# Kernel optimization log

Measured on AMD Instinct MI355X. Metric: run time of the kernel, lower is better.

Reference implementation:

```python
import jax, jax.numpy as jnp
import numpy as np

EPS = 1e-5


def _gcn_conv(h, W, b, src, dst, norm, N):
    # h: (B, N, F_in) -> linear transform then normalized neighbor aggregation
    h = h @ W                                  # (B, N, H)
    msg = h[:, src, :] * norm[None, :, None]   # gather + edge norm, (B, E, H)
    agg = jax.vmap(lambda m: jax.ops.segment_sum(m, dst, num_segments=N))(msg)
    return agg + b


def _batchnorm(h, gamma, beta):
    # BatchNorm1d over flattened (B*N, H), training-mode batch statistics
    B, N, H = h.shape
    f = h.reshape(-1, H)
    mean = f.mean(axis=0)
    var = f.var(axis=0)
    f = (f - mean) * jax.lax.rsqrt(var + EPS) * gamma + beta
    return f.reshape(B, N, H)


def setup_inputs() -> dict:
    key = jax.random.key(0)
    ks = jax.random.split(key, 6)
    B, N, E, IN, H, OUT = 2, 20000, 640000, 128, 128, 10
    x = jax.random.normal(ks[0], (B, N, IN), dtype=jnp.float32)
    edge_index = jax.random.randint(ks[1], (2, E), 0, N, dtype=jnp.int64)
    W1 = jax.random.normal(ks[2], (IN, H), dtype=jnp.float32) / np.sqrt(IN)
    W2 = jax.random.normal(ks[3], (H, H), dtype=jnp.float32) / np.sqrt(H)
    Wc = jax.random.normal(ks[4], (H, OUT), dtype=jnp.float32) / np.sqrt(H)
    return {
        "x": x,
        "W1": W1, "b1": jnp.zeros((H,), jnp.float32),
        "W2": W2, "b2": jnp.zeros((H,), jnp.float32),
        "g1": jnp.ones((H,), jnp.float32), "bt1": jnp.zeros((H,), jnp.float32),
        "g2": jnp.ones((H,), jnp.float32), "bt2": jnp.zeros((H,), jnp.float32),
        "Wc": Wc, "bc": jnp.zeros((OUT,), jnp.float32),
        "edge_index": edge_index,
    }


def reference(x, W1, b1, W2, b2, g1, bt1, g2, bt2, Wc, bc, edge_index):
    N = x.shape[1]
    loops = jnp.arange(N, dtype=edge_index.dtype)
    src = jnp.concatenate([edge_index[0], loops])  # add self-loops (GCNConv default)
    dst = jnp.concatenate([edge_index[1], loops])
    deg = jax.ops.segment_sum(jnp.ones(src.shape[0], x.dtype), dst, num_segments=N)
    dinv = jnp.where(deg > 0, jax.lax.rsqrt(deg), 0.0)
    norm = dinv[src] * dinv[dst]                   # symmetric GCN normalization

    h = jax.nn.relu(_gcn_conv(x, W1, b1, src, dst, norm, N))
    h = _batchnorm(h, g1, bt1)
    # dropout is identity in eval mode
    h = jax.nn.relu(_gcn_conv(h, W2, b2, src, dst, norm, N))
    h = _batchnorm(h, g2, bt2)
    return h @ Wc + bc                              # (B, N, out_dim)
```

## Files before the change

### kernel.cpp

```cpp
#include <hip/hip_runtime.h>
#include <hip/hip_bf16.h>


constexpr int Nn   = 20000;
constexpr int Ee   = 640000;
constexpr int OUTd = 10;
constexpr int Mm   = 2 * Nn;
constexpr int ELLW = 96;
constexpr int NSLOT = 64;
constexpr int NP   = 8;
constexpr int PSZ  = Nn / NP;
constexpr int PCAP = 98304;
constexpr int GMB  = Mm / 64;
constexpr int BKB  = (Ee + 1023) / 1024;
constexpr int PBB  = 96;
#define EPSV 1e-5f
constexpr float INV_M = 1.0f / (float)Mm;

using frag16 = __attribute__((ext_vector_type(8))) short;
using f32x4  = __attribute__((ext_vector_type(4))) float;

__device__ inline short bf(float f) {
    union { __hip_bfloat16 h; short s; } u;
    u.h = __float2bfloat16(f);
    return u.s;
}
__device__ inline float lo16(unsigned u) { union { unsigned v; float f; } x; x.v = u << 16;        return x.f; }
__device__ inline float hi16(unsigned u) { union { unsigned v; float f; } x; x.v = u & 0xffff0000u; return x.f; }
__device__ inline unsigned pack2(float f0, float f1) {
    return (unsigned)(unsigned short)bf(f0) | ((unsigned)(unsigned short)bf(f1) << 16);
}
__device__ inline float wdeg(int c) { return rsqrtf((float)c + 1.0f); }

__global__ __launch_bounds__(256) void fg1_k(const int* __restrict__ src, const int* __restrict__ dst,
                                             int* __restrict__ cursor, uint2* __restrict__ pairs,
                                             const float* __restrict__ A,
                                             const float* __restrict__ W,
                                             unsigned short* __restrict__ Hout) {
    __shared__ short Wl[128 * 136];
    __shared__ int pcnt[NP];
    __shared__ int pbase[NP];
    int t = threadIdx.x;

    if (blockIdx.x >= GMB) {
        int s  = blockIdx.x - GMB;
        int e0 = s * 1024;
        if (t < NP) pcnt[t] = 0;
        __syncthreads();
        int es[4], ed[4], pp[4], pos[4];
        #pragma unroll
        for (int it = 0; it < 4; ++it) {
            int e = e0 + it * 256 + t;
            int d = dst[e];
            es[it] = src[e];
            ed[it] = d;
            pp[it] = (int)((unsigned)d / (unsigned)PSZ);
            pos[it] = atomicAdd(&pcnt[pp[it]], 1);
        }
        __syncthreads();
        if (t < NP) pbase[t] = atomicAdd(&cursor[t], pcnt[t]);
        __syncthreads();
        #pragma unroll
        for (int it = 0; it < 4; ++it) {
            int idx = pbase[pp[it]] + pos[it];
            if (idx < PCAP)
                pairs[(size_t)pp[it] * PCAP + idx] = make_uint2((unsigned)es[it], (unsigned)ed[it]);
        }
        return;
    }

    int bid = blockIdx.x;

    for (int it = 0; it < 8; ++it) {
        int lin = it * 256 + t;
        int kp  = lin & 63;
        int n4  = (lin >> 6) * 4;
        float4 w0 = *(const float4*)(W + (size_t)(2 * kp) * 128 + n4);
        float4 w1 = *(const float4*)(W + (size_t)(2 * kp + 1) * 128 + n4);
        *(unsigned*)&Wl[(n4 + 0) * 136 + 2 * kp] = pack2(w0.x, w1.x);
        *(unsigned*)&Wl[(n4 + 1) * 136 + 2 * kp] = pack2(w0.y, w1.y);
        *(unsigned*)&Wl[(n4 + 2) * 136 + 2 * kp] = pack2(w0.z, w1.z);
        *(unsigned*)&Wl[(n4 + 3) * 136 + 2 * kp] = pack2(w0.w, w1.w);
    }
    __syncthreads();

    int wv = t >> 6, l = t & 63;
    int row_q = l >> 4, lane16 = l & 15;
    int row0 = bid * 64 + wv * 16;

    frag16 a[4];
    const float* Arow = A + (size_t)(row0 + lane16) * 128;
    #pragma unroll
    for (int q = 0; q < 4; ++q) {
        int k0 = q * 32 + row_q * 8;
        float4 v0 = *(const float4*)(Arow + k0);
        float4 v1 = *(const float4*)(Arow + k0 + 4);
        frag16 fa = { bf(v0.x), bf(v0.y), bf(v0.z), bf(v0.w),
                      bf(v1.x), bf(v1.y), bf(v1.z), bf(v1.w) };
        a[q] = fa;
    }

    f32x4 acc[8];
    #pragma unroll
    for (int c = 0; c < 8; ++c) acc[c] = (f32x4){0.f, 0.f, 0.f, 0.f};

    #pragma unroll
    for (int c = 0; c < 8; ++c) {
        int n = c * 16 + lane16;
        #pragma unroll
        for (int q = 0; q < 4; ++q) {
            int k0 = q * 32 + row_q * 8;
            frag16 b = *(const frag16*)&Wl[n * 136 + k0];
            acc[c] = __builtin_amdgcn_mfma_f32_16x16x32_bf16(a[q], b, acc[c], 0, 0, 0);
        }
    }

    #pragma unroll
    for (int r = 0; r < 4; ++r) {
        int rg = row0 + row_q * 4 + r;
        int b  = rg >= Nn;
        int n  = rg - b * Nn;
        unsigned short* dstp = Hout + (size_t)n * 256 + b * 128;
        #pragma unroll
        for (int c = 0; c < 8; ++c)
            dstp[c * 16 + lane16] = (unsigned short)bf(acc[c][r]);
    }
}

__global__ __launch_bounds__(256) void scat2_k(const uint2* __restrict__ pairs,
                                               const int* __restrict__ cursor,
                                               int* __restrict__ cnt, int* __restrict__ ell) {
    int p     = blockIdx.x & (NP - 1);
    int chunk = blockIdx.x >> 3;
    int m = cursor[p]; if (m > PCAP) m = PCAP;
    const uint2* bk = pairs + (size_t)p * PCAP;
    for (int i = chunk * 256 + threadIdx.x; i < m; i += PBB * 256) {
        uint2 pr = bk[i];
        int d = (int)pr.y;
        int pos = atomicAdd(&cnt[d], 1);
        if (pos < ELLW) ell[(size_t)d * ELLW + pos] = (int)pr.x;
    }
}

__global__ __launch_bounds__(256) void gemm2_k(const unsigned short* __restrict__ Abf,
                                               const float* __restrict__ W,
                                               const float* __restrict__ g,
                                               const float* __restrict__ bt,
                                               const float* __restrict__ S,
                                               const int* __restrict__ cnt,
                                               unsigned short* __restrict__ Hout) {
    __shared__ short Wl[128 * 136];
    __shared__ float al[128], cl[128], dpart[2][128];
    int t = threadIdx.x;

    if (t < 128) {
        float s = 0.f, ss = 0.f;
        #pragma unroll 8
        for (int k = 0; k < NSLOT; ++k) {
            s  += S[k * 256 + t];
            ss += S[k * 256 + 128 + t];
        }
        float m   = s * INV_M;
        float var = ss * INV_M - m * m;
        float a   = g[t] * rsqrtf(var + EPSV);
        float c   = bt[t] - m * a;
        al[t] = a; cl[t] = c;
    }
    __syncthreads();

    for (int it = 0; it < 8; ++it) {
        int lin = it * 256 + t;
        int kp  = lin & 63;
        int n4  = (lin >> 6) * 4;
        float a0 = al[2 * kp], a1 = al[2 * kp + 1];
        float4 w0 = *(const float4*)(W + (size_t)(2 * kp) * 128 + n4);
        float4 w1 = *(const float4*)(W + (size_t)(2 * kp + 1) * 128 + n4);
        w0.x *= a0; w0.y *= a0; w0.z *= a0; w0.w *= a0;
        w1.x *= a1; w1.y *= a1; w1.z *= a1; w1.w *= a1;
        *(unsigned*)&Wl[(n4 + 0) * 136 + 2 * kp] = pack2(w0.x, w1.x);
        *(unsigned*)&Wl[(n4 + 1) * 136 + 2 * kp] = pack2(w0.y, w1.y);
        *(unsigned*)&Wl[(n4 + 2) * 136 + 2 * kp] = pack2(w0.z, w1.z);
        *(unsigned*)&Wl[(n4 + 3) * 136 + 2 * kp] = pack2(w0.w, w1.w);
    }

    {
        int col = t & 127, hh = t >> 7;
        const float* Wc0 = W + (size_t)(hh * 64) * 128 + col;
        float dp = 0.f;
        #pragma unroll 8
        for (int k = 0; k < 64; ++k) dp += cl[hh * 64 + k] * Wc0[(size_t)k * 128];
        dpart[hh][col] = dp;
    }
    __syncthreads();

    int wv = t >> 6, l = t & 63;
    int row_q = l >> 4, lane16 = l & 15;
    int row0 = blockIdx.x * 64 + wv * 16;

    int rgA = row0 + lane16;
    int bA  = rgA >= Nn;
    int nA  = rgA - bA * Nn;
    const unsigned short* Arow = Abf + (size_t)nA * 256 + bA * 128;
    frag16 a[4];
    #pragma unroll
    for (int q = 0; q < 4; ++q) {
        int k0 = q * 32 + row_q * 8;
        a[q] = *(const frag16*)(Arow + k0);
    }

    f32x4 acc[8];
    #pragma unroll
    for (int c = 0; c < 8; ++c) {
        int n = c * 16 + lane16;
        float d = dpart[0][n] + dpart[1][n];
        acc[c] = (f32x4){d, d, d, d};
    }

    #pragma unroll
    for (int c = 0; c < 8; ++c) {
        int n = c * 16 + lane16;
        #pragma unroll
        for (int q = 0; q < 4; ++q) {
            int k0 = q * 32 + row_q * 8;
            frag16 b = *(const frag16*)&Wl[n * 136 + k0];
            acc[c] = __builtin_amdgcn_mfma_f32_16x16x32_bf16(a[q], b, acc[c], 0, 0, 0);
        }
    }

    #pragma unroll
    for (int r = 0; r < 4; ++r) {
        int rg = row0 + row_q * 4 + r;
        int b  = rg >= Nn;
        int n  = rg - b * Nn;
        float dv = wdeg(cnt[n]);
        unsigned short* dst = Hout + (size_t)n * 256 + b * 128;
        #pragma unroll
        for (int c = 0; c < 8; ++c)
            dst[c * 16 + lane16] = (unsigned short)bf(acc[c][r] * dv);
    }
}

template<int WEIGHTED>
__global__ __launch_bounds__(256) void aggs_k(const unsigned short* __restrict__ h,
                                              const int* __restrict__ ell,
                                              const int* __restrict__ cnt,
                                              const float* __restrict__ bias,
                                              unsigned short* __restrict__ act,
                                              float* __restrict__ S) {
    int t    = threadIdx.x;
    int wv   = t >> 6;
    int l    = t & 63;
    int p    = blockIdx.x & 7;
    int ng   = blockIdx.x >> 3;
    int esub = l >> 2;
    int c4   = l & 3;
    int uo   = p * 4 + c4;
    const uint4* h4 = (const uint4*)h;
    int cb   = (p & 3) * 32 + c4 * 8;

    float oS[8] = {0.f,0.f,0.f,0.f,0.f,0.f,0.f,0.f};
    float qS[8] = {0.f,0.f,0.f,0.f,0.f,0.f,0.f,0.f};

    for (int s = 0; s < 2; ++s) {
        int n = __builtin_amdgcn_readfirstlane(ng * 8 + wv * 2 + s);
        int degc = cnt[n];
        float dn = wdeg(degc);
        int deg = degc > ELLW ? ELLW : degc;
        const int* row = ell + (size_t)n * ELLW;

        uint4 u = h4[(size_t)n * 32 + uo];

        float a0 = 0.f, a1 = 0.f, a2 = 0.f, a3 = 0.f;
        float a4 = 0.f, a5 = 0.f, a6 = 0.f, a7 = 0.f;

        int j = 0;
        for (; j + 32 <= deg; j += 32) {
            int i0 = row[j + esub];
            int i1 = row[j + 16 + esub];
            float w0 = 1.f, w1 = 1.f;
            if (WEIGHTED) { w0 = wdeg(cnt[i0]); w1 = wdeg(cnt[i1]); }
            uint4 v0 = h4[(size_t)i0 * 32 + uo];
            uint4 v1 = h4[(size_t)i1 * 32 + uo];
            if (WEIGHTED) {
                a0 = fmaf(w0, lo16(v0.x), a0); a1 = fmaf(w0, hi16(v0.x), a1);
                a2 = fmaf(w0, lo16(v0.y), a2); a3 = fmaf(w0, hi16(v0.y), a3);
                a4 = fmaf(w0, lo16(v0.z), a4); a5 = fmaf(w0, hi16(v0.z), a5);
                a6 = fmaf(w0, lo16(v0.w), a6); a7 = fmaf(w0, hi16(v0.w), a7);
                a0 = fmaf(w1, lo16(v1.x), a0); a1 = fmaf(w1, hi16(v1.x), a1);
                a2 = fmaf(w1, lo16(v1.y), a2); a3 = fmaf(w1, hi16(v1.y), a3);
                a4 = fmaf(w1, lo16(v1.z), a4); a5 = fmaf(w1, hi16(v1.z), a5);
                a6 = fmaf(w1, lo16(v1.w), a6); a7 = fmaf(w1, hi16(v1.w), a7);
            } else {
                a0 += lo16(v0.x); a1 += hi16(v0.x); a2 += lo16(v0.y); a3 += hi16(v0.y);
                a4 += lo16(v0.z); a5 += hi16(v0.z); a6 += lo16(v0.w); a7 += hi16(v0.w);
                a0 += lo16(v1.x); a1 += hi16(v1.x); a2 += lo16(v1.y); a3 += hi16(v1.y);
                a4 += lo16(v1.z); a5 += hi16(v1.z); a6 += lo16(v1.w); a7 += hi16(v1.w);
            }
        }
        for (; j + 16 <= deg; j += 16) {
            int i0 = row[j + esub];
            float w0 = 1.f;
            if (WEIGHTED) w0 = wdeg(cnt[i0]);
            uint4 v0 = h4[(size_t)i0 * 32 + uo];
            if (WEIGHTED) {
                a0 = fmaf(w0, lo16(v0.x), a0); a1 = fmaf(w0, hi16(v0.x), a1);
                a2 = fmaf(w0, lo16(v0.y), a2); a3 = fmaf(w0, hi16(v0.y), a3);
                a4 = fmaf(w0, lo16(v0.z), a4); a5 = fmaf(w0, hi16(v0.z), a5);
                a6 = fmaf(w0, lo16(v0.w), a6); a7 = fmaf(w0, hi16(v0.w), a7);
            } else {
                a0 += lo16(v0.x); a1 += hi16(v0.x); a2 += lo16(v0.y); a3 += hi16(v0.y);
                a4 += lo16(v0.z); a5 += hi16(v0.z); a6 += lo16(v0.w); a7 += hi16(v0.w);
            }
        }
        if (j < deg) {
            int e = j + esub;
            if (e < deg) {
                int i0 = row[e];
                float w0 = 1.f;
                if (WEIGHTED) w0 = wdeg(cnt[i0]);
                uint4 v0 = h4[(size_t)i0 * 32 + uo];
                if (WEIGHTED) {
                    a0 = fmaf(w0, lo16(v0.x), a0); a1 = fmaf(w0, hi16(v0.x), a1);
                    a2 = fmaf(w0, lo16(v0.y), a2); a3 = fmaf(w0, hi16(v0.y), a3);
                    a4 = fmaf(w0, lo16(v0.z), a4); a5 = fmaf(w0, hi16(v0.z), a5);
                    a6 = fmaf(w0, lo16(v0.w), a6); a7 = fmaf(w0, hi16(v0.w), a7);
                } else {
                    a0 += lo16(v0.x); a1 += hi16(v0.x); a2 += lo16(v0.y); a3 += hi16(v0.y);
                    a4 += lo16(v0.z); a5 += hi16(v0.z); a6 += lo16(v0.w); a7 += hi16(v0.w);
                }
            }
        }

        #pragma unroll
        for (int m = 4; m <= 32; m <<= 1) {
            a0 += __shfl_xor(a0, m); a1 += __shfl_xor(a1, m);
            a2 += __shfl_xor(a2, m); a3 += __shfl_xor(a3, m);
            a4 += __shfl_xor(a4, m); a5 += __shfl_xor(a5, m);
            a6 += __shfl_xor(a6, m); a7 += __shfl_xor(a7, m);
        }

        if (l < 4) {
            float4 b0 = *(const float4*)(bias + cb);
            float4 b1 = *(const float4*)(bias + cb + 4);
            float o0, o1, o2, o3, o4, o5, o6, o7;
            if (WEIGHTED) {
                o0 = fmaxf(fmaf(dn, fmaf(dn, lo16(u.x), a0), b0.x), 0.f);
                o1 = fmaxf(fmaf(dn, fmaf(dn, hi16(u.x), a1), b0.y), 0.f);
                o2 = fmaxf(fmaf(dn, fmaf(dn, lo16(u.y), a2), b0.z), 0.f);
                o3 = fmaxf(fmaf(dn, fmaf(dn, hi16(u.y), a3), b0.w), 0.f);
                o4 = fmaxf(fmaf(dn, fmaf(dn, lo16(u.z), a4), b1.x), 0.f);
                o5 = fmaxf(fmaf(dn, fmaf(dn, hi16(u.z), a5), b1.y), 0.f);
                o6 = fmaxf(fmaf(dn, fmaf(dn, lo16(u.w), a6), b1.z), 0.f);
                o7 = fmaxf(fmaf(dn, fmaf(dn, hi16(u.w), a7), b1.w), 0.f);
            } else {
                o0 = fmaxf(fmaf(dn, a0 + lo16(u.x), b0.x), 0.f);
                o1 = fmaxf(fmaf(dn, a1 + hi16(u.x), b0.y), 0.f);
                o2 = fmaxf(fmaf(dn, a2 + lo16(u.y), b0.z), 0.f);
                o3 = fmaxf(fmaf(dn, a3 + hi16(u.y), b0.w), 0.f);
                o4 = fmaxf(fmaf(dn, a4 + lo16(u.z), b1.x), 0.f);
                o5 = fmaxf(fmaf(dn, a5 + hi16(u.z), b1.y), 0.f);
                o6 = fmaxf(fmaf(dn, a6 + lo16(u.w), b1.z), 0.f);
                o7 = fmaxf(fmaf(dn, a7 + hi16(u.w), b1.w), 0.f);
            }
            uint4 st;
            st.x = pack2(o0, o1); st.y = pack2(o2, o3);
            st.z = pack2(o4, o5); st.w = pack2(o6, o7);
            *(uint4*)(act + (size_t)n * 256 + (size_t)p * 32 + (size_t)c4 * 8) = st;

            oS[0] += o0; oS[1] += o1; oS[2] += o2; oS[3] += o3;
            oS[4] += o4; oS[5] += o5; oS[6] += o6; oS[7] += o7;
            qS[0] += o0*o0; qS[1] += o1*o1; qS[2] += o2*o2; qS[3] += o3*o3;
            qS[4] += o4*o4; qS[5] += o5*o5; qS[6] += o6*o6; qS[7] += o7*o7;
        }
    }

    __shared__ float sh[4][4][16];
    if (l < 4) {
        float* ptr = sh[wv][l];
        #pragma unroll
        for (int k = 0; k < 8; ++k) { ptr[k] = oS[k]; ptr[8 + k] = qS[k]; }
    }
    __syncthreads();
    if (t < 64) {
        int c = t >> 4;
        int k = t & 15;
        float v = sh[0][c][k] + sh[1][c][k] + sh[2][c][k] + sh[3][c][k];
        int col  = (p & 3) * 32 + c * 8 + (k & 7);
        int stat = k >> 3;
        atomicAdd(&S[((blockIdx.x >> 3) & (NSLOT - 1)) * 256 + stat * 128 + col], v);
    }
}

__global__ __launch_bounds__(256) void gemmout_k(const unsigned short* __restrict__ act,
                                                 const float* __restrict__ Wc,
                                                 const float* __restrict__ bc,
                                                 const float* __restrict__ g,
                                                 const float* __restrict__ bt,
                                                 const float* __restrict__ S,
                                                 float* __restrict__ out) {
    __shared__ float Wl[128 * OUTd];
    __shared__ float bl[OUTd];
    __shared__ float al[128], cl[128];
    int t = threadIdx.x;
    for (int i = t; i < 128 * OUTd; i += 256) Wl[i] = Wc[i];
    if (t < OUTd) bl[t] = bc[t];
    if (t < 128) {
        float s = 0.f, ss = 0.f;
        #pragma unroll 8
        for (int k = 0; k < NSLOT; ++k) {
            s  += S[k * 256 + t];
            ss += S[k * 256 + 128 + t];
        }
        float m   = s * INV_M;
        float var = ss * INV_M - m * m;
        float a   = g[t] * rsqrtf(var + EPSV);
        al[t] = a;
        cl[t] = bt[t] - m * a;
    }
    __syncthreads();

    int r = blockIdx.x * 256 + t;
    if (r >= Mm) return;
    int b = r >= Nn;
    int n = r - b * Nn;

    float acc[OUTd];
    #pragma unroll
    for (int jj = 0; jj < OUTd; jj++) acc[jj] = 0.f;

    const uint4* a4 = (const uint4*)(act + (size_t)n * 256 + b * 128);
    #pragma unroll 4
    for (int k4 = 0; k4 < 16; k4++) {
        uint4 u = a4[k4];
        int k = k4 * 8;
        float e0 = lo16(u.x) * al[k+0] + cl[k+0];
        float e1 = hi16(u.x) * al[k+1] + cl[k+1];
        float e2 = lo16(u.y) * al[k+2] + cl[k+2];
        float e3 = hi16(u.y) * al[k+3] + cl[k+3];
        float e4 = lo16(u.z) * al[k+4] + cl[k+4];
        float e5 = hi16(u.z) * al[k+5] + cl[k+5];
        float e6 = lo16(u.w) * al[k+6] + cl[k+6];
        float e7 = hi16(u.w) * al[k+7] + cl[k+7];
        #pragma unroll
        for (int jj = 0; jj < OUTd; jj++) {
            acc[jj] += e0 * Wl[(k+0) * OUTd + jj];
            acc[jj] += e1 * Wl[(k+1) * OUTd + jj];
            acc[jj] += e2 * Wl[(k+2) * OUTd + jj];
            acc[jj] += e3 * Wl[(k+3) * OUTd + jj];
            acc[jj] += e4 * Wl[(k+4) * OUTd + jj];
            acc[jj] += e5 * Wl[(k+5) * OUTd + jj];
            acc[jj] += e6 * Wl[(k+6) * OUTd + jj];
            acc[jj] += e7 * Wl[(k+7) * OUTd + jj];
        }
    }
    #pragma unroll
    for (int jj = 0; jj < OUTd; jj++) out[(size_t)r * OUTd + jj] = acc[jj] + bl[jj];
}

extern "C" void kernel_launch(void* const* d_in, const int* in_sizes, int n_in,
                              void* d_out, int out_size, void* d_ws, size_t ws_size,
                              hipStream_t stream) {
    (void)in_sizes; (void)n_in; (void)out_size; (void)ws_size;

    const float* x   = (const float*)d_in[0];
    const float* W1  = (const float*)d_in[1];
    const float* b1  = (const float*)d_in[2];
    const float* W2  = (const float*)d_in[3];
    const float* b2  = (const float*)d_in[4];
    const float* g1  = (const float*)d_in[5];
    const float* bt1 = (const float*)d_in[6];
    const float* g2  = (const float*)d_in[7];
    const float* bt2 = (const float*)d_in[8];
    const float* Wc  = (const float*)d_in[9];
    const float* bc  = (const float*)d_in[10];
    const int*   ei  = (const int*)d_in[11];
    const int* srcp = ei;
    const int* dstp = ei + Ee;

    char* ws = (char*)d_ws;
    size_t off = 0;
    auto alloc = [&](size_t bytes) -> void* {
        void* p = ws + off;
        off += (bytes + 511) & ~(size_t)511;
        return p;
    };
    unsigned short* h   = (unsigned short*)alloc((size_t)Mm * 128 * 2);
    unsigned short* act = (unsigned short*)alloc((size_t)Mm * 128 * 2);
    int*   cnt  = (int*)alloc(Nn * 4 + 2 * NSLOT * 256 * 4 + NP * 4);
    float* S1   = (float*)(cnt + Nn);
    float* S2   = S1 + NSLOT * 256;
    int*   cursor = (int*)(S2 + NSLOT * 256);
    int*   ell  = (int*)alloc((size_t)Nn * ELLW * 4);
    uint2* pairs = (uint2*)alloc((size_t)NP * PCAP * 8);

    float* out = (float*)d_out;

    hipMemsetAsync(cnt, 0, Nn * 4 + 2 * NSLOT * 256 * 4 + NP * 4, stream);
    fg1_k<<<GMB + BKB, 256, 0, stream>>>(srcp, dstp, cursor, pairs, x, W1, h);

    scat2_k<<<NP * PBB, 256, 0, stream>>>(pairs, cursor, cnt, ell);

    aggs_k<1><<<(Nn / 8) * 8, 256, 0, stream>>>(h, ell, cnt, b1, act, S1);

    gemm2_k<<<Mm / 64, 256, 0, stream>>>(act, W2, g1, bt1, S1, cnt, h);
    aggs_k<0><<<(Nn / 8) * 8, 256, 0, stream>>>(h, ell, cnt, b2, act, S2);

    gemmout_k<<<(Mm + 255) / 256, 256, 0, stream>>>(act, Wc, bc, g2, bt2, S2, out);
}
```

Before: 296.5 us.

## Remap aggregation warps to one node and 64 columns each, unroll edge loop

Reworks the SpMM aggregation kernel so each block splits its 256 columns into 4 parts instead of 8, with each warp owning one node and 8 lanes spanning 64 bf16 columns (128 bytes per neighbor row). The edge loop now issues four gathers per iteration instead of two. The aim is fewer, wider gather transactions per neighbor, fewer redundant index loads across blocks, and more memory-level parallelism. In exchange each block handles fewer nodes, there is one more shuffle-free lane group, and per-block stats atomics roughly double in count.

```diff
diff --git a/kernel.cpp b/kernel.cpp
--- a/kernel.cpp
+++ b/kernel.cpp
@@ -240,6 +240,17 @@
     }
 }
 
+#define ACCW8(V, W) \
+    a0 = fmaf(W, lo16((V).x), a0); a1 = fmaf(W, hi16((V).x), a1); \
+    a2 = fmaf(W, lo16((V).y), a2); a3 = fmaf(W, hi16((V).y), a3); \
+    a4 = fmaf(W, lo16((V).z), a4); a5 = fmaf(W, hi16((V).z), a5); \
+    a6 = fmaf(W, lo16((V).w), a6); a7 = fmaf(W, hi16((V).w), a7);
+#define ACC8(V) \
+    a0 += lo16((V).x); a1 += hi16((V).x); \
+    a2 += lo16((V).y); a3 += hi16((V).y); \
+    a4 += lo16((V).z); a5 += hi16((V).z); \
+    a6 += lo16((V).w); a7 += hi16((V).w);
+
 template<int WEIGHTED>
 __global__ __launch_bounds__(256) void aggs_k(const unsigned short* __restrict__ h,
                                               const int* __restrict__ ell,
@@ -247,147 +258,110 @@
                                               const float* __restrict__ bias,
                                               unsigned short* __restrict__ act,
                                               float* __restrict__ S) {
-    int t    = threadIdx.x;
-    int wv   = t >> 6;
-    int l    = t & 63;
-    int p    = blockIdx.x & 7;
-    int ng   = blockIdx.x >> 3;
-    int esub = l >> 2;
-    int c4   = l & 3;
-    int uo   = p * 4 + c4;
+    int t  = threadIdx.x;
+    int wv = t >> 6;
+    int l  = t & 63;
+    int p  = blockIdx.x & 3;
+    int ng = blockIdx.x >> 2;
+    int n  = __builtin_amdgcn_readfirstlane(ng * 4 + wv);
+    int c  = l & 7;
+    int eo = l >> 3;
+    int uo = p * 8 + c;
     const uint4* h4 = (const uint4*)h;
-    int cb   = (p & 3) * 32 + c4 * 8;
-
-    float oS[8] = {0.f,0.f,0.f,0.f,0.f,0.f,0.f,0.f};
-    float qS[8] = {0.f,0.f,0.f,0.f,0.f,0.f,0.f,0.f};
-
-    for (int s = 0; s < 2; ++s) {
-        int n = __builtin_amdgcn_readfirstlane(ng * 8 + wv * 2 + s);
-        int degc = cnt[n];
-        float dn = wdeg(degc);
-        int deg = degc > ELLW ? ELLW : degc;
-        const int* row = ell + (size_t)n * ELLW;
-
-        uint4 u = h4[(size_t)n * 32 + uo];
-
-        float a0 = 0.f, a1 = 0.f, a2 = 0.f, a3 = 0.f;
-        float a4 = 0.f, a5 = 0.f, a6 = 0.f, a7 = 0.f;
-
-        int j = 0;
-        for (; j + 32 <= deg; j += 32) {
-            int i0 = row[j + esub];
-            int i1 = row[j + 16 + esub];
-            float w0 = 1.f, w1 = 1.f;
-            if (WEIGHTED) { w0 = wdeg(cnt[i0]); w1 = wdeg(cnt[i1]); }
-            uint4 v0 = h4[(size_t)i0 * 32 + uo];
-            uint4 v1 = h4[(size_t)i1 * 32 + uo];
-            if (WEIGHTED) {
-                a0 = fmaf(w0, lo16(v0.x), a0); a1 = fmaf(w0, hi16(v0.x), a1);
-                a2 = fmaf(w0, lo16(v0.y), a2); a3 = fmaf(w0, hi16(v0.y), a3);
-                a4 = fmaf(w0, lo16(v0.z), a4); a5 = fmaf(w0, hi16(v0.z), a5);
-                a6 = fmaf(w0, lo16(v0.w), a6); a7 = fmaf(w0, hi16(v0.w), a7);
-                a0 = fmaf(w1, lo16(v1.x), a0); a1 = fmaf(w1, hi16(v1.x), a1);
-                a2 = fmaf(w1, lo16(v1.y), a2); a3 = fmaf(w1, hi16(v1.y), a3);
-                a4 = fmaf(w1, lo16(v1.z), a4); a5 = fmaf(w1, hi16(v1.z), a5);
-                a6 = fmaf(w1, lo16(v1.w), a6); a7 = fmaf(w1, hi16(v1.w), a7);
-            } else {
-                a0 += lo16(v0.x); a1 += hi16(v0.x); a2 += lo16(v0.y); a3 += hi16(v0.y);
-                a4 += lo16(v0.z); a5 += hi16(v0.z); a6 += lo16(v0.w); a7 += hi16(v0.w);
-                a0 += lo16(v1.x); a1 += hi16(v1.x); a2 += lo16(v1.y); a3 += hi16(v1.y);
-                a4 += lo16(v1.z); a5 += hi16(v1.z); a6 += lo16(v1.w); a7 += hi16(v1.w);
-            }
-        }
-        for (; j + 16 <= deg; j += 16) {
-            int i0 = row[j + esub];
-            float w0 = 1.f;
-            if (WEIGHTED) w0 = wdeg(cnt[i0]);
-            uint4 v0 = h4[(size_t)i0 * 32 + uo];
-            if (WEIGHTED) {
-                a0 = fmaf(w0, lo16(v0.x), a0); a1 = fmaf(w0, hi16(v0.x), a1);
-                a2 = fmaf(w0, lo16(v0.y), a2); a3 = fmaf(w0, hi16(v0.y), a3);
-                a4 = fmaf(w0, lo16(v0.z), a4); a5 = fmaf(w0, hi16(v0.z), a5);
-                a6 = fmaf(w0, lo16(v0.w), a6); a7 = fmaf(w0, hi16(v0.w), a7);
-            } else {
-                a0 += lo16(v0.x); a1 += hi16(v0.x); a2 += lo16(v0.y); a3 += hi16(v0.y);
-                a4 += lo16(v0.z); a5 += hi16(v0.z); a6 += lo16(v0.w); a7 += hi16(v0.w);
-            }
-        }
-        if (j < deg) {
-            int e = j + esub;
-            if (e < deg) {
-                int i0 = row[e];
-                float w0 = 1.f;
-                if (WEIGHTED) w0 = wdeg(cnt[i0]);
-                uint4 v0 = h4[(size_t)i0 * 32 + uo];
-                if (WEIGHTED) {
-                    a0 = fmaf(w0, lo16(v0.x), a0); a1 = fmaf(w0, hi16(v0.x), a1);
-                    a2 = fmaf(w0, lo16(v0.y), a2); a3 = fmaf(w0, hi16(v0.y), a3);
-                    a4 = fmaf(w0, lo16(v0.z), a4); a5 = fmaf(w0, hi16(v0.z), a5);
-                    a6 = fmaf(w0, lo16(v0.w), a6); a7 = fmaf(w0, hi16(v0.w), a7);
-                } else {
-                    a0 += lo16(v0.x); a1 += hi16(v0.x); a2 += lo16(v0.y); a3 += hi16(v0.y);
-                    a4 += lo16(v0.z); a5 += hi16(v0.z); a6 += lo16(v0.w); a7 += hi16(v0.w);
-                }
-            }
-        }
-
-        #pragma unroll
-        for (int m = 4; m <= 32; m <<= 1) {
-            a0 += __shfl_xor(a0, m); a1 += __shfl_xor(a1, m);
-            a2 += __shfl_xor(a2, m); a3 += __shfl_xor(a3, m);
-            a4 += __shfl_xor(a4, m); a5 += __shfl_xor(a5, m);
-            a6 += __shfl_xor(a6, m); a7 += __shfl_xor(a7, m);
-        }
-
-        if (l < 4) {
-            float4 b0 = *(const float4*)(bias + cb);
-            float4 b1 = *(const float4*)(bias + cb + 4);
-            float o0, o1, o2, o3, o4, o5, o6, o7;
-            if (WEIGHTED) {
-                o0 = fmaxf(fmaf(dn, fmaf(dn, lo16(u.x), a0), b0.x), 0.f);
-                o1 = fmaxf(fmaf(dn, fmaf(dn, hi16(u.x), a1), b0.y), 0.f);
-                o2 = fmaxf(fmaf(dn, fmaf(dn, lo16(u.y), a2), b0.z), 0.f);
-                o3 = fmaxf(fmaf(dn, fmaf(dn, hi16(u.y), a3), b0.w), 0.f);
-                o4 = fmaxf(fmaf(dn, fmaf(dn, lo16(u.z), a4), b1.x), 0.f);
-                o5 = fmaxf(fmaf(dn, fmaf(dn, hi16(u.z), a5), b1.y), 0.f);
-                o6 = fmaxf(fmaf(dn, fmaf(dn, lo16(u.w), a6), b1.z), 0.f);
-                o7 = fmaxf(fmaf(dn, fmaf(dn, hi16(u.w), a7), b1.w), 0.f);
-            } else {
-                o0 = fmaxf(fmaf(dn, a0 + lo16(u.x), b0.x), 0.f);
-                o1 = fmaxf(fmaf(dn, a1 + hi16(u.x), b0.y), 0.f);
-                o2 = fmaxf(fmaf(dn, a2 + lo16(u.y), b0.z), 0.f);
-                o3 = fmaxf(fmaf(dn, a3 + hi16(u.y), b0.w), 0.f);
-                o4 = fmaxf(fmaf(dn, a4 + lo16(u.z), b1.x), 0.f);
-                o5 = fmaxf(fmaf(dn, a5 + hi16(u.z), b1.y), 0.f);
-                o6 = fmaxf(fmaf(dn, a6 + lo16(u.w), b1.z), 0.f);
-                o7 = fmaxf(fmaf(dn, a7 + hi16(u.w), b1.w), 0.f);
-            }
-            uint4 st;
-            st.x = pack2(o0, o1); st.y = pack2(o2, o3);
-            st.z = pack2(o4, o5); st.w = pack2(o6, o7);
-            *(uint4*)(act + (size_t)n * 256 + (size_t)p * 32 + (size_t)c4 * 8) = st;
-
-            oS[0] += o0; oS[1] += o1; oS[2] += o2; oS[3] += o3;
-            oS[4] += o4; oS[5] += o5; oS[6] += o6; oS[7] += o7;
-            qS[0] += o0*o0; qS[1] += o1*o1; qS[2] += o2*o2; qS[3] += o3*o3;
-            qS[4] += o4*o4; qS[5] += o5*o5; qS[6] += o6*o6; qS[7] += o7*o7;
-        }
-    }
-
-    __shared__ float sh[4][4][16];
-    if (l < 4) {
+
+    int degc = cnt[n];
+    float dn = wdeg(degc);
+    int deg = degc > ELLW ? ELLW : degc;
+    const int* row = ell + (size_t)n * ELLW;
+
+    uint4 u = h4[(size_t)n * 32 + uo];
+
+    float a0 = 0.f, a1 = 0.f, a2 = 0.f, a3 = 0.f;
+    float a4 = 0.f, a5 = 0.f, a6 = 0.f, a7 = 0.f;
+
+    int j = 0;
+    for (; j + 32 <= deg; j += 32) {
+        int i0 = row[j      + eo];
+        int i1 = row[j +  8 + eo];
+        int i2 = row[j + 16 + eo];
+        int i3 = row[j + 24 + eo];
+        uint4 v0 = h4[(size_t)i0 * 32 + uo];
+        uint4 v1 = h4[(size_t)i1 * 32 + uo];
+        uint4 v2 = h4[(size_t)i2 * 32 + uo];
+        uint4 v3 = h4[(size_t)i3 * 32 + uo];
+        if (WEIGHTED) {
+            float w0 = wdeg(cnt[i0]), w1 = wdeg(cnt[i1]);
+            float w2 = wdeg(cnt[i2]), w3 = wdeg(cnt[i3]);
+            ACCW8(v0, w0); ACCW8(v1, w1); ACCW8(v2, w2); ACCW8(v3, w3);
+        } else {
+            ACC8(v0); ACC8(v1); ACC8(v2); ACC8(v3);
+        }
+    }
+    for (; j + 8 <= deg; j += 8) {
+        int i0 = row[j + eo];
+        uint4 v0 = h4[(size_t)i0 * 32 + uo];
+        if (WEIGHTED) { float w0 = wdeg(cnt[i0]); ACCW8(v0, w0); }
+        else          { ACC8(v0); }
+    }
+    if (j + eo < deg) {
+        int i0 = row[j + eo];
+        uint4 v0 = h4[(size_t)i0 * 32 + uo];
+        if (WEIGHTED) { float w0 = wdeg(cnt[i0]); ACCW8(v0, w0); }
+        else          { ACC8(v0); }
+    }
+
+    #pragma unroll
+    for (int m = 8; m <= 32; m <<= 1) {
+        a0 += __shfl_xor(a0, m); a1 += __shfl_xor(a1, m);
+        a2 += __shfl_xor(a2, m); a3 += __shfl_xor(a3, m);
+        a4 += __shfl_xor(a4, m); a5 += __shfl_xor(a5, m);
+        a6 += __shfl_xor(a6, m); a7 += __shfl_xor(a7, m);
+    }
+
+    __shared__ float sh[4][8][16];
+    if (l < 8) {
+        int colbase = (p & 1) * 64 + l * 8;
+        float4 b0 = *(const float4*)(bias + colbase);
+        float4 b1 = *(const float4*)(bias + colbase + 4);
+        float o0, o1, o2, o3, o4, o5, o6, o7;
+        if (WEIGHTED) {
+            o0 = fmaxf(fmaf(dn, fmaf(dn, lo16(u.x), a0), b0.x), 0.f);
+            o1 = fmaxf(fmaf(dn, fmaf(dn, hi16(u.x), a1), b0.y), 0.f);
+            o2 = fmaxf(fmaf(dn, fmaf(dn, lo16(u.y), a2), b0.z), 0.f);
+            o3 = fmaxf(fmaf(dn, fmaf(dn, hi16(u.y), a3), b0.w), 0.f);
+            o4 = fmaxf(fmaf(dn, fmaf(dn, lo16(u.z), a4), b1.x), 0.f);
+            o5 = fmaxf(fmaf(dn, fmaf(dn, hi16(u.z), a5), b1.y), 0.f);
+            o6 = fmaxf(fmaf(dn, fmaf(dn, lo16(u.w), a6), b1.z), 0.f);
+            o7 = fmaxf(fmaf(dn, fmaf(dn, hi16(u.w), a7), b1.w), 0.f);
+        } else {
+            o0 = fmaxf(fmaf(dn, a0 + lo16(u.x), b0.x), 0.f);
+            o1 = fmaxf(fmaf(dn, a1 + hi16(u.x), b0.y), 0.f);
+            o2 = fmaxf(fmaf(dn, a2 + lo16(u.y), b0.z), 0.f);
+            o3 = fmaxf(fmaf(dn, a3 + hi16(u.y), b0.w), 0.f);
+            o4 = fmaxf(fmaf(dn, a4 + lo16(u.z), b1.x), 0.f);
+            o5 = fmaxf(fmaf(dn, a5 + hi16(u.z), b1.y), 0.f);
+            o6 = fmaxf(fmaf(dn, a6 + lo16(u.w), b1.z), 0.f);
+            o7 = fmaxf(fmaf(dn, a7 + hi16(u.w), b1.w), 0.f);
+        }
+        uint4 st;
+        st.x = pack2(o0, o1); st.y = pack2(o2, o3);
+        st.z = pack2(o4, o5); st.w = pack2(o6, o7);
+        *(uint4*)(act + (size_t)n * 256 + (size_t)p * 64 + (size_t)l * 8) = st;
+
         float* ptr = sh[wv][l];
-        #pragma unroll
-        for (int k = 0; k < 8; ++k) { ptr[k] = oS[k]; ptr[8 + k] = qS[k]; }
+        ptr[0] = o0; ptr[1] = o1; ptr[2] = o2; ptr[3] = o3;
+        ptr[4] = o4; ptr[5] = o5; ptr[6] = o6; ptr[7] = o7;
+        ptr[8]  = o0*o0; ptr[9]  = o1*o1; ptr[10] = o2*o2; ptr[11] = o3*o3;
+        ptr[12] = o4*o4; ptr[13] = o5*o5; ptr[14] = o6*o6; ptr[15] = o7*o7;
     }
     __syncthreads();
-    if (t < 64) {
-        int c = t >> 4;
-        int k = t & 15;
-        float v = sh[0][c][k] + sh[1][c][k] + sh[2][c][k] + sh[3][c][k];
-        int col  = (p & 3) * 32 + c * 8 + (k & 7);
+    if (t < 128) {
+        int gi = t >> 4;
+        int k  = t & 15;
+        float v = sh[0][gi][k] + sh[1][gi][k] + sh[2][gi][k] + sh[3][gi][k];
+        int col  = (p & 1) * 64 + gi * 8 + (k & 7);
         int stat = k >> 3;
-        atomicAdd(&S[((blockIdx.x >> 3) & (NSLOT - 1)) * 256 + stat * 128 + col], v);
+        atomicAdd(&S[((blockIdx.x >> 2) & (NSLOT - 1)) * 256 + stat * 128 + col], v);
     }
 }
 
@@ -500,10 +474,10 @@
 
     scat2_k<<<NP * PBB, 256, 0, stream>>>(pairs, cursor, cnt, ell);
 
-    aggs_k<1><<<(Nn / 8) * 8, 256, 0, stream>>>(h, ell, cnt, b1, act, S1);
+    aggs_k<1><<<(Nn / 4) * 4, 256, 0, stream>>>(h, ell, cnt, b1, act, S1);
 
     gemm2_k<<<Mm / 64, 256, 0, stream>>>(act, W2, g1, bt1, S1, cnt, h);
-    aggs_k<0><<<(Nn / 8) * 8, 256, 0, stream>>>(h, ell, cnt, b2, act, S2);
+    aggs_k<0><<<(Nn / 4) * 4, 256, 0, stream>>>(h, ell, cnt, b2, act, S2);
 
     gemmout_k<<<(Mm + 255) / 256, 256, 0, stream>>>(act, Wc, bc, g2, bt2, S2, out);
 }
```

Result: faster. 251.4 us (-15.2%).
